# Kernel tuning notes

Measured on AMD Instinct MI355X. Metric: run time of the kernel, lower is better.

Reference implementation:

```python
import jax, jax.numpy as jnp
import numpy as np

TOKENS = 8192
HIDDEN = 6144
NUM_EXPERTS = 768  # n_routed_experts (512) + zero_expert_num (256)
TOP_K = 12
ROUTED_SCALING_FACTOR = 2.5


def setup_inputs() -> dict:
    key = jax.random.key(0)
    k1, k2, k3 = jax.random.split(key, 3)
    hidden_states = jax.random.normal(k1, (TOKENS, HIDDEN), dtype=jnp.float32)
    classifier_weight = jax.random.normal(k2, (NUM_EXPERTS, HIDDEN), dtype=jnp.float32) * (1.0 / np.sqrt(HIDDEN))
    e_score_correction_bias = jax.random.normal(k3, (NUM_EXPERTS,), dtype=jnp.float32) * 0.1
    return {
        "hidden_states": hidden_states,
        "classifier_weight": classifier_weight,
        "e_score_correction_bias": e_score_correction_bias,
    }


def reference(hidden_states, classifier_weight, e_score_correction_bias):
    # [T, H] -> router logits [T, E] in fp32 (source casts to float32)
    x = hidden_states.reshape(-1, HIDDEN).astype(jnp.float32)
    router_logits = jnp.einsum('th,eh->te', x, classifier_weight)

    # npu_moe_gating_top_k(renorm=0, norm_type=0): softmax scores,
    # bias-corrected selection, gather un-biased scores, scale.
    scores = jax.nn.softmax(router_logits, axis=-1)                # [T, E]
    scores_for_choice = scores + e_score_correction_bias[None, :]  # [T, E]
    _, topk_indices = jax.lax.top_k(scores_for_choice, TOP_K)       # [T, K]
    topk_weights = jnp.take_along_axis(scores, topk_indices, axis=-1)
    topk_weights = topk_weights * ROUTED_SCALING_FACTOR

    return topk_indices.astype(jnp.int32), topk_weights
```

## Files before the change

kernel.cpp:

```cpp
#include <hip/hip_runtime.h>

#define TOKENS  8192
#define HIDDEN  6144
#define EXPERTS 768
#define TOPK    12
#define RSF     2.5f
#define ROWH    (HIDDEN * 2)

typedef float    f4 __attribute__((ext_vector_type(4)));
typedef _Float16 h8 __attribute__((ext_vector_type(8)));
typedef _Float16 h2 __attribute__((ext_vector_type(2)));
typedef __fp16   g2 __attribute__((ext_vector_type(2)));

#define BM 128
#define BN 96
#define BK 64
#define NKT (HIDDEN / BK)
#define LO_SCALE 4096.0f
#define LO_INV   2.44140625e-4f

static __device__ inline h2 pk(float a, float b) {
    g2 r = __builtin_amdgcn_cvt_pkrtz(a, b);
    return __builtin_bit_cast(h2, r);
}

static __device__ inline void cvt8(const f4 a, const f4 b, h8& hi, h8& lo) {
    h2 ha = pk(a.x, a.y), hb = pk(a.z, a.w), hc = pk(b.x, b.y), hd = pk(b.z, b.w);
    h2 la = pk((a.x - (float)ha[0]) * LO_SCALE, (a.y - (float)ha[1]) * LO_SCALE);
    h2 lb = pk((a.z - (float)hb[0]) * LO_SCALE, (a.w - (float)hb[1]) * LO_SCALE);
    h2 lc = pk((b.x - (float)hc[0]) * LO_SCALE, (b.y - (float)hc[1]) * LO_SCALE);
    h2 ld = pk((b.z - (float)hd[0]) * LO_SCALE, (b.w - (float)hd[1]) * LO_SCALE);
    hi[0]=ha[0]; hi[1]=ha[1]; hi[2]=hb[0]; hi[3]=hb[1];
    hi[4]=hc[0]; hi[5]=hc[1]; hi[6]=hd[0]; hi[7]=hd[1];
    lo[0]=la[0]; lo[1]=la[1]; lo[2]=lb[0]; lo[3]=lb[1];
    lo[4]=lc[0]; lo[5]=lc[1]; lo[6]=ld[0]; lo[7]=ld[1];
}

__global__ __launch_bounds__(256)
void split_convert(float* __restrict__ X, float* __restrict__ W) {
    const size_t GX = (size_t)TOKENS * HIDDEN / 8;
    const size_t GW = (size_t)EXPERTS * HIDDEN / 8;
    size_t gid = (size_t)blockIdx.x * 256 + threadIdx.x;
    if (gid >= GX + GW) return;
    float* base; size_t loc;
    if (gid < GX) { base = X; loc = gid; } else { base = W; loc = gid - GX; }
    const f4* p = (const f4*)(base + loc * 8);
    f4 a = p[0], b = p[1];
    h8 hi, lo;
    cvt8(a, b, hi, lo);
    h8* o = (h8*)(base + loc * 8);
    o[0] = hi; o[1] = lo;
}

typedef __attribute__((address_space(1))) const void av1;
typedef __attribute__((address_space(3))) void av3;
static __device__ inline void stage16(const void* g, void* l) {
    __builtin_amdgcn_global_load_lds((av1*)g, (av3*)l, 16, 0, 0);
}

__global__ __launch_bounds__(256, 2)
void router_gemm(const _Float16* __restrict__ Xs, const _Float16* __restrict__ Ws,
                 float* __restrict__ L) {
    __shared__ _Float16 sm[224 * 64 * 2];

    const int t    = threadIdx.x;
    const int bm   = blockIdx.y * BM;
    const int bn   = blockIdx.x * BN;
    const int lane = t & 63;
    const int w    = t >> 6;
    const int lr   = lane & 15;
    const int lq   = lane >> 4;

    const int isLo = w >> 1;
    const int jb   = (w & 1) * 14;
    const int lr8  = lane >> 3;
    const int gs   = lane & 7;

    const _Float16* ps[14];
    uint32_t        ldso[14];
#pragma unroll
    for (int q = 0; q < 14; ++q) {
        const int j = jb + q;
        const int r = j * 8 + lr8;
        const int g = gs ^ (r & 7);
        const _Float16* row = (r < BM) ? (Xs + (size_t)(bm + r) * ROWH)
                                       : (Ws + (size_t)(bn + r - BM) * ROWH);
        ps[q]   = row + g * 16 + isLo * 8;
        ldso[q] = (uint32_t)(isLo * 14336 + j * 512);
    }

    uint32_t aoff[4][2], boff[3][2];
#pragma unroll
    for (int mi = 0; mi < 4; ++mi) {
        const int r = (w & 1) * 64 + mi * 16 + lr;
#pragma unroll
        for (int ks = 0; ks < 2; ++ks)
            aoff[mi][ks] = r * 64 + (((ks * 4 + lq) ^ (r & 7)) * 8);
    }
#pragma unroll
    for (int ni = 0; ni < 3; ++ni) {
        const int r = 128 + (w >> 1) * 48 + ni * 16 + lr;
#pragma unroll
        for (int ks = 0; ks < 2; ++ks)
            boff[ni][ks] = r * 64 + (((ks * 4 + lq) ^ (r & 7)) * 8);
    }

    f4 acc_h[4][3], acc_c[4][3];
#pragma unroll
    for (int i = 0; i < 4; ++i)
#pragma unroll
        for (int j = 0; j < 3; ++j) { acc_h[i][j] = f4{0,0,0,0}; acc_c[i][j] = f4{0,0,0,0}; }

    for (int T = 0; T < NKT; ++T) {
        __syncthreads();
#pragma unroll
        for (int q = 0; q < 14; ++q) {
            stage16((const void*)ps[q], (void*)(sm + ldso[q]));
            ps[q] += 128;
        }
        __syncthreads();

#pragma unroll
        for (int ks = 0; ks < 2; ++ks) {
            h8 ah[4], al[4], bh[3], bl[3];
#pragma unroll
            for (int mi = 0; mi < 4; ++mi) {
                ah[mi] = *(const h8*)(sm + aoff[mi][ks]);
                al[mi] = *(const h8*)(sm + aoff[mi][ks] + 14336);
            }
#pragma unroll
            for (int ni = 0; ni < 3; ++ni) {
                bh[ni] = *(const h8*)(sm + boff[ni][ks]);
                bl[ni] = *(const h8*)(sm + boff[ni][ks] + 14336);
            }
#pragma unroll
            for (int mi = 0; mi < 4; ++mi)
#pragma unroll
                for (int ni = 0; ni < 3; ++ni) {
                    acc_h[mi][ni] = __builtin_amdgcn_mfma_f32_16x16x32_f16(ah[mi], bh[ni], acc_h[mi][ni], 0, 0, 0);
                    acc_c[mi][ni] = __builtin_amdgcn_mfma_f32_16x16x32_f16(ah[mi], bl[ni], acc_c[mi][ni], 0, 0, 0);
                    acc_c[mi][ni] = __builtin_amdgcn_mfma_f32_16x16x32_f16(al[mi], bh[ni], acc_c[mi][ni], 0, 0, 0);
                }
        }
    }

#pragma unroll
    for (int mi = 0; mi < 4; ++mi)
#pragma unroll
        for (int ni = 0; ni < 3; ++ni)
#pragma unroll
            for (int r = 0; r < 4; ++r) {
                const int gm = bm + (w & 1) * 64 + mi * 16 + lq * 4 + r;
                const int gn = bn + (w >> 1) * 48 + ni * 16 + lr;
                L[(size_t)gm * EXPERTS + gn] = acc_h[mi][ni][r] + acc_c[mi][ni][r] * LO_INV;
            }
}

__global__ __launch_bounds__(256)
void router_topk(const float* __restrict__ L, const float* __restrict__ bias,
                 float* __restrict__ outIdx, float* __restrict__ outW) {
    __shared__ float sb[EXPERTS];
    const int t = threadIdx.x;
    for (int i = t; i < EXPERTS; i += 256) sb[i] = bias[i];
    __syncthreads();

    const int lane  = t & 63;
    const int wave  = t >> 6;
    const int token = blockIdx.x * 4 + wave;
    const float* row = L + (size_t)token * EXPERTS;

    float lg[12];
#pragma unroll
    for (int j = 0; j < 12; ++j) lg[j] = row[lane + 64 * j];

    float m = lg[0];
#pragma unroll
    for (int j = 1; j < 12; ++j) m = fmaxf(m, lg[j]);
#pragma unroll
    for (int o = 32; o > 0; o >>= 1) m = fmaxf(m, __shfl_xor(m, o));

    float s = 0.0f;
#pragma unroll
    for (int j = 0; j < 12; ++j) { lg[j] = __expf(lg[j] - m); s += lg[j]; }
#pragma unroll
    for (int o = 32; o > 0; o >>= 1) s += __shfl_xor(s, o);
    const float inv = 1.0f / s;

    float cand[12];
#pragma unroll
    for (int j = 0; j < 12; ++j) {
        lg[j] *= inv;
        cand[j] = lg[j] + sb[lane + 64 * j];
    }

#pragma unroll
    for (int r = 0; r < TOPK; ++r) {
        float bv = -__builtin_inff();
        int   bi = EXPERTS;
#pragma unroll
        for (int j = 0; j < 12; ++j) {
            const int e = lane + 64 * j;
            const bool better = (cand[j] > bv) || (cand[j] == bv && e < bi);
            bv = better ? cand[j] : bv;
            bi = better ? e : bi;
        }
#pragma unroll
        for (int o = 32; o > 0; o >>= 1) {
            const float ov = __shfl_xor(bv, o);
            const int   oi = __shfl_xor(bi, o);
            const bool better = (ov > bv) || (ov == bv && oi < bi);
            bv = better ? ov : bv;
            bi = better ? oi : bi;
        }
        if (lane == 0) {
            outIdx[token * TOPK + r] = (float)bi;
            outW  [token * TOPK + r] = (bv - sb[bi]) * RSF;
        }
        if ((bi & 63) == lane) {
            const int slot = bi >> 6;
#pragma unroll
            for (int j = 0; j < 12; ++j)
                if (j == slot) cand[j] = -__builtin_inff();
        }
    }
}

extern "C" void kernel_launch(void* const* d_in, const int* in_sizes, int n_in,
                              void* d_out, int out_size, void* d_ws, size_t ws_size,
                              hipStream_t stream) {
    float* X = (float*)d_in[0];
    float* W = (float*)d_in[1];
    const float* B = (const float*)d_in[2];

    float* logits = (float*)d_ws;
    float* outIdx = (float*)d_out;
    float* outW   = outIdx + (size_t)TOKENS * TOPK;

    const int ngroups = (TOKENS + EXPERTS) * HIDDEN / 8;
    split_convert<<<ngroups / 256, 256, 0, stream>>>(X, W);

    dim3 grid_gemm(EXPERTS / BN, TOKENS / BM);
    router_gemm<<<grid_gemm, 256, 0, stream>>>((const _Float16*)X, (const _Float16*)W, logits);
    router_topk<<<TOKENS / 4, 256, 0, stream>>>(logits, B, outIdx, outW);
}
```

Before: 545.9 us.

## Double-buffer router GEMM LDS staging with a smaller K tile

Result: no change. 544.1 us (-0.3%).

```diff
diff --git a/kernel.cpp b/kernel.cpp
--- a/kernel.cpp
+++ b/kernel.cpp
@@ -14,8 +14,10 @@
 
 #define BM 128
 #define BN 96
-#define BK 64
+#define BK 32
 #define NKT (HIDDEN / BK)
+#define BUFH 14336
+#define LOH  7168
 #define LO_SCALE 4096.0f
 #define LO_INV   2.44140625e-4f
 
@@ -61,7 +63,7 @@
 __global__ __launch_bounds__(256, 2)
 void router_gemm(const _Float16* __restrict__ Xs, const _Float16* __restrict__ Ws,
                  float* __restrict__ L) {
-    __shared__ _Float16 sm[224 * 64 * 2];
+    __shared__ _Float16 sm[2 * BUFH];
 
     const int t    = threadIdx.x;
     const int bm   = blockIdx.y * BM;
@@ -71,38 +73,32 @@
     const int lr   = lane & 15;
     const int lq   = lane >> 4;
 
-    const int isLo = w >> 1;
-    const int jb   = (w & 1) * 14;
-    const int lr8  = lane >> 3;
-    const int gs   = lane & 7;
-
-    const _Float16* ps[14];
-    uint32_t        ldso[14];
-#pragma unroll
-    for (int q = 0; q < 14; ++q) {
-        const int j = jb + q;
-        const int r = j * 8 + lr8;
-        const int g = gs ^ (r & 7);
+    const _Float16* ps[7];
+    uint32_t        ldso[7];
+#pragma unroll
+    for (int q = 0; q < 7; ++q) {
+        const int j    = w * 7 + q;
+        const int isLo = (j >= 14);
+        const int jj   = isLo ? j - 14 : j;
+        const int r    = jj * 16 + (lane >> 2);
+        const int p    = lane & 3;
+        const int g    = p ^ (r & 3);
         const _Float16* row = (r < BM) ? (Xs + (size_t)(bm + r) * ROWH)
                                        : (Ws + (size_t)(bn + r - BM) * ROWH);
         ps[q]   = row + g * 16 + isLo * 8;
-        ldso[q] = (uint32_t)(isLo * 14336 + j * 512);
-    }
-
-    uint32_t aoff[4][2], boff[3][2];
+        ldso[q] = (uint32_t)(isLo * LOH + jj * 512);
+    }
+
+    uint32_t aoff[4], boff[3];
 #pragma unroll
     for (int mi = 0; mi < 4; ++mi) {
         const int r = (w & 1) * 64 + mi * 16 + lr;
-#pragma unroll
-        for (int ks = 0; ks < 2; ++ks)
-            aoff[mi][ks] = r * 64 + (((ks * 4 + lq) ^ (r & 7)) * 8);
+        aoff[mi] = r * 32 + ((lq ^ (r & 3)) * 8);
     }
 #pragma unroll
     for (int ni = 0; ni < 3; ++ni) {
         const int r = 128 + (w >> 1) * 48 + ni * 16 + lr;
-#pragma unroll
-        for (int ks = 0; ks < 2; ++ks)
-            boff[ni][ks] = r * 64 + (((ks * 4 + lq) ^ (r & 7)) * 8);
+        boff[ni] = r * 32 + ((lq ^ (r & 3)) * 8);
     }
 
     f4 acc_h[4][3], acc_c[4][3];
@@ -111,37 +107,46 @@
 #pragma unroll
         for (int j = 0; j < 3; ++j) { acc_h[i][j] = f4{0,0,0,0}; acc_c[i][j] = f4{0,0,0,0}; }
 
-    for (int T = 0; T < NKT; ++T) {
+#pragma unroll
+    for (int q = 0; q < 7; ++q) {
+        stage16((const void*)ps[q], (void*)(sm + ldso[q]));
+        ps[q] += 64;
+    }
+
+    auto do_tile = [&](const uint32_t boR, const uint32_t boW, const bool doStage) {
+        if (doStage) {
+#pragma unroll
+            for (int q = 0; q < 7; ++q) {
+                stage16((const void*)ps[q], (void*)(sm + boW + ldso[q]));
+                ps[q] += 64;
+            }
+        }
+        h8 ah[4], al[4], bh[3], bl[3];
+#pragma unroll
+        for (int mi = 0; mi < 4; ++mi) {
+            ah[mi] = *(const h8*)(sm + boR + aoff[mi]);
+            al[mi] = *(const h8*)(sm + boR + aoff[mi] + LOH);
+        }
+#pragma unroll
+        for (int ni = 0; ni < 3; ++ni) {
+            bh[ni] = *(const h8*)(sm + boR + boff[ni]);
+            bl[ni] = *(const h8*)(sm + boR + boff[ni] + LOH);
+        }
+#pragma unroll
+        for (int mi = 0; mi < 4; ++mi)
+#pragma unroll
+            for (int ni = 0; ni < 3; ++ni) {
+                acc_h[mi][ni] = __builtin_amdgcn_mfma_f32_16x16x32_f16(ah[mi], bh[ni], acc_h[mi][ni], 0, 0, 0);
+                acc_c[mi][ni] = __builtin_amdgcn_mfma_f32_16x16x32_f16(ah[mi], bl[ni], acc_c[mi][ni], 0, 0, 0);
+                acc_c[mi][ni] = __builtin_amdgcn_mfma_f32_16x16x32_f16(al[mi], bh[ni], acc_c[mi][ni], 0, 0, 0);
+            }
+    };
+
+    for (int T2 = 0; T2 < NKT / 2; ++T2) {
         __syncthreads();
-#pragma unroll
-        for (int q = 0; q < 14; ++q) {
-            stage16((const void*)ps[q], (void*)(sm + ldso[q]));
-            ps[q] += 128;
-        }
+        do_tile(0u, (uint32_t)BUFH, true);
         __syncthreads();
-
-#pragma unroll
-        for (int ks = 0; ks < 2; ++ks) {
-            h8 ah[4], al[4], bh[3], bl[3];
-#pragma unroll
-            for (int mi = 0; mi < 4; ++mi) {
-                ah[mi] = *(const h8*)(sm + aoff[mi][ks]);
-                al[mi] = *(const h8*)(sm + aoff[mi][ks] + 14336);
-            }
-#pragma unroll
-            for (int ni = 0; ni < 3; ++ni) {
-                bh[ni] = *(const h8*)(sm + boff[ni][ks]);
-                bl[ni] = *(const h8*)(sm + boff[ni][ks] + 14336);
-            }
-#pragma unroll
-            for (int mi = 0; mi < 4; ++mi)
-#pragma unroll
-                for (int ni = 0; ni < 3; ++ni) {
-                    acc_h[mi][ni] = __builtin_amdgcn_mfma_f32_16x16x32_f16(ah[mi], bh[ni], acc_h[mi][ni], 0, 0, 0);
-                    acc_c[mi][ni] = __builtin_amdgcn_mfma_f32_16x16x32_f16(ah[mi], bl[ni], acc_c[mi][ni], 0, 0, 0);
-                    acc_c[mi][ni] = __builtin_amdgcn_mfma_f32_16x16x32_f16(al[mi], bh[ni], acc_c[mi][ni], 0, 0, 0);
-                }
-        }
+        do_tile((uint32_t)BUFH, 0u, T2 != NKT / 2 - 1);
     }
 
 #pragma unroll
```
